# Kernel tuning notes

Measured on AMD Instinct MI355X. Metric: run time of the kernel, lower is better.

The kernel has to match this reference:

```python
import jax, jax.numpy as jnp
import numpy as np

HIDDEN = 128
N_NODES = 100000
N_EDGES = 200000
NEG_SLOPE = 0.01  # torch LeakyReLU default


def setup_inputs() -> dict:
    key = jax.random.key(0)
    ks = jax.random.split(key, 12)
    h = HIDDEN
    lim = 1.0 / np.sqrt(h)
    lim3 = 1.0 / np.sqrt(3 * h)
    u = lambda k, shape, l: jax.random.uniform(k, shape, jnp.float32, -l, l)
    return {
        "x_src": jax.random.normal(ks[0], (N_NODES, h), jnp.float32),
        "x_dst": jax.random.normal(ks[1], (N_NODES, h), jnp.float32),
        "edge_index": jax.random.randint(ks[2], (2, N_EDGES), 0, N_NODES, jnp.int64),
        # parent_encoder Linear(h, h)
        "Wp": u(ks[3], (h, h), lim), "bp": u(ks[4], (h,), lim),
        # child_encoder Linear(h, h)
        "Wc": u(ks[5], (h, h), lim), "bc": u(ks[6], (h,), lim),
        # edge_weight_mlp: Linear(3h, h) -> ReLU -> Linear(h, h)
        "W1": u(ks[7], (h, 3 * h), lim3), "b1": u(ks[8], (h,), lim3),
        "W2": u(ks[9], (h, h), lim), "b2": u(ks[10], (h,), lim),
    }


def reference(x_src, x_dst, edge_index, Wp, bp, Wc, bc, W1, b1, W2, b2):
    # gather node feats per edge  [E, h]
    par = x_src[edge_index[0]]
    cld = x_dst[edge_index[1]]
    # dual encoders: Linear + LeakyReLU (Dropout is identity in eval)
    enc_p = jax.nn.leaky_relu(par @ Wp.T + bp, NEG_SLOPE)
    enc_c = jax.nn.leaky_relu(cld @ Wc.T + bc, NEG_SLOPE)
    diff = jnp.abs(par - cld)
    ef = jnp.concatenate([enc_p, enc_c, diff], axis=-1)  # [E, 3h]
    # edge_weight_mlp
    edge_attr = jax.nn.relu(ef @ W1.T + b1) @ W2.T + b2  # [E, h]
    return edge_attr
```

## Files before the change

### kernel.cpp

```cpp
#include <hip/hip_runtime.h>

typedef unsigned short u16;
typedef __attribute__((ext_vector_type(8))) short v8s;
typedef __attribute__((ext_vector_type(4))) float v4f;
typedef __attribute__((ext_vector_type(4))) float f4;

#define HID 128
#define TM  64
#define EFS 392
#define HS  136
#define FOS 136

__device__ __forceinline__ u16 f2b(float f) {
    union { float f; unsigned u; } v; v.f = f;
    unsigned u = v.u;
    u += 0x7fffu + ((u >> 16) & 1u);
    return (u16)(u >> 16);
}

#define MFMA(A, B, C) __builtin_amdgcn_mfma_f32_16x16x32_bf16(A, B, C, 0, 0, 0)

__global__ void cvt_weights(const float* __restrict__ Wp, const float* __restrict__ Wc,
                            const float* __restrict__ W1, const float* __restrict__ W2,
                            u16* __restrict__ dst)
{
    int i = blockIdx.x * 256 + threadIdx.x;
    const float* s; int off;
    if (i < 4096)       { s = Wp; off = 0; }
    else if (i < 8192)  { s = Wc; off = 4096; }
    else if (i < 20480) { s = W1; off = 8192; }
    else                { s = W2; off = 20480; }
    int j = i - off;
    f4 v = ((const f4*)s)[j];
    u16* d = dst + (size_t)i * 4;
    d[0] = f2b(v[0]); d[1] = f2b(v[1]); d[2] = f2b(v[2]); d[3] = f2b(v[3]);
}

__global__ __launch_bounds__(256, 2) void edge_attr_kernel(
    const float* __restrict__ x_src, const float* __restrict__ x_dst,
    const int* __restrict__ ei,
    const u16* __restrict__ wsW,
    const float* __restrict__ bp, const float* __restrict__ bc,
    const float* __restrict__ b1, const float* __restrict__ b2,
    float* __restrict__ out, int E)
{
    __shared__ __align__(16) u16 sEF[TM * EFS];
    __shared__ __align__(16) u16 sH [TM * HS];

    const u16* wsWp = wsW;
    const u16* wsWc = wsW + 16384;
    const u16* wsW1 = wsW + 32768;
    const u16* wsW2 = wsW + 81920;

    const int t  = threadIdx.x;
    const int e0 = blockIdx.x * TM;
    const int* ei0 = ei;
    const int* ei1 = ei + E;

    #pragma unroll
    for (int i = 0; i < 4; ++i) {
        int idx = t + i * 256;
        int r = idx >> 4;
        int c = (idx & 15) << 3;
        int e = e0 + r; if (e >= E) e = E - 1;
        const f4* ps = (const f4*)(x_src + (size_t)ei0[e] * HID + c);
        const f4* qs = (const f4*)(x_dst + (size_t)ei1[e] * HID + c);
        f4 p0 = ps[0], p1 = ps[1];
        f4 q0 = qs[0], q1 = qs[1];
        v8s pb, qb, db;
        #pragma unroll
        for (int j = 0; j < 4; ++j) {
            pb[j]     = (short)f2b(p0[j]);
            pb[j + 4] = (short)f2b(p1[j]);
            qb[j]     = (short)f2b(q0[j]);
            qb[j + 4] = (short)f2b(q1[j]);
            db[j]     = (short)f2b(fabsf(p0[j] - q0[j]));
            db[j + 4] = (short)f2b(fabsf(p1[j] - q1[j]));
        }
        *(v8s*)&sEF[r * EFS       + c] = pb;
        *(v8s*)&sEF[r * EFS + 128 + c] = qb;
        *(v8s*)&sEF[r * EFS + 256 + c] = db;
    }
    __syncthreads();

    const int lane = t & 63;
    const int ln = lane & 15;
    const int lq = lane >> 4;
    const int n0 = (t >> 6) * 32;

    {
        v8s Bp[2][4], Bc[2][4];
        float bpv[2], bcv[2];
        #pragma unroll
        for (int nt = 0; nt < 2; ++nt) {
            int n = n0 + nt * 16 + ln;
            bpv[nt] = bp[n];
            bcv[nt] = bc[n];
            #pragma unroll
            for (int kt = 0; kt < 4; ++kt) {
                Bp[nt][kt] = *(const v8s*)(wsWp + (size_t)n * HID + kt * 32 + lq * 8);
                Bc[nt][kt] = *(const v8s*)(wsWc + (size_t)n * HID + kt * 32 + lq * 8);
            }
        }
        v4f aP[4][2], aC[4][2];
        #pragma unroll
        for (int mt = 0; mt < 4; ++mt)
            #pragma unroll
            for (int nt = 0; nt < 2; ++nt) {
                aP[mt][nt] = (v4f){0.f, 0.f, 0.f, 0.f};
                aC[mt][nt] = (v4f){0.f, 0.f, 0.f, 0.f};
            }
        #pragma unroll
        for (int mt = 0; mt < 4; ++mt) {
            const int rbase = (mt * 16 + ln) * EFS + lq * 8;
            v8s A[4];
            #pragma unroll
            for (int kt = 0; kt < 4; ++kt) A[kt] = *(const v8s*)&sEF[rbase + kt * 32];
            #pragma unroll
            for (int nt = 0; nt < 2; ++nt)
                #pragma unroll
                for (int kt = 0; kt < 4; ++kt) aP[mt][nt] = MFMA(A[kt], Bp[nt][kt], aP[mt][nt]);
            #pragma unroll
            for (int kt = 0; kt < 4; ++kt) A[kt] = *(const v8s*)&sEF[rbase + 128 + kt * 32];
            #pragma unroll
            for (int nt = 0; nt < 2; ++nt)
                #pragma unroll
                for (int kt = 0; kt < 4; ++kt) aC[mt][nt] = MFMA(A[kt], Bc[nt][kt], aC[mt][nt]);
        }
        __syncthreads();
        #pragma unroll
        for (int mt = 0; mt < 4; ++mt)
            #pragma unroll
            for (int nt = 0; nt < 2; ++nt)
                #pragma unroll
                for (int rg = 0; rg < 4; ++rg) {
                    int row = mt * 16 + lq * 4 + rg;
                    int col = n0 + nt * 16 + ln;
                    float vp = aP[mt][nt][rg] + bpv[nt];
                    vp = vp > 0.f ? vp : 0.01f * vp;
                    sEF[row * EFS + col] = f2b(vp);
                    float vc = aC[mt][nt][rg] + bcv[nt];
                    vc = vc > 0.f ? vc : 0.01f * vc;
                    sEF[row * EFS + 128 + col] = f2b(vc);
                }
        __syncthreads();
    }

    {
        float b1v[2];
        #pragma unroll
        for (int nt = 0; nt < 2; ++nt) b1v[nt] = b1[n0 + nt * 16 + ln];
        v4f acc[4][2];
        #pragma unroll
        for (int mt = 0; mt < 4; ++mt)
            #pragma unroll
            for (int nt = 0; nt < 2; ++nt) acc[mt][nt] = (v4f){0.f, 0.f, 0.f, 0.f};
        #pragma unroll
        for (int ktc = 0; ktc < 3; ++ktc) {
            v8s B[2][4];
            #pragma unroll
            for (int nt = 0; nt < 2; ++nt) {
                int n = n0 + nt * 16 + ln;
                #pragma unroll
                for (int k4 = 0; k4 < 4; ++k4)
                    B[nt][k4] = *(const v8s*)(wsW1 + (size_t)n * 384 + ktc * 128 + k4 * 32 + lq * 8);
            }
            #pragma unroll
            for (int mt = 0; mt < 4; ++mt) {
                const int rbase = (mt * 16 + ln) * EFS + ktc * 128 + lq * 8;
                v8s A[4];
                #pragma unroll
                for (int k4 = 0; k4 < 4; ++k4) A[k4] = *(const v8s*)&sEF[rbase + k4 * 32];
                #pragma unroll
                for (int nt = 0; nt < 2; ++nt)
                    #pragma unroll
                    for (int k4 = 0; k4 < 4; ++k4) acc[mt][nt] = MFMA(A[k4], B[nt][k4], acc[mt][nt]);
            }
        }
        #pragma unroll
        for (int mt = 0; mt < 4; ++mt)
            #pragma unroll
            for (int nt = 0; nt < 2; ++nt)
                #pragma unroll
                for (int rg = 0; rg < 4; ++rg) {
                    int row = mt * 16 + lq * 4 + rg;
                    int col = n0 + nt * 16 + ln;
                    float v = acc[mt][nt][rg] + b1v[nt];
                    sH[row * HS + col] = f2b(fmaxf(v, 0.f));
                }
        __syncthreads();
    }

    {
        float* sF = (float*)sEF;
        v8s B2[2][4];
        float b2v[2];
        #pragma unroll
        for (int nt = 0; nt < 2; ++nt) {
            int n = n0 + nt * 16 + ln;
            b2v[nt] = b2[n];
            #pragma unroll
            for (int kt = 0; kt < 4; ++kt)
                B2[nt][kt] = *(const v8s*)(wsW2 + (size_t)n * HID + kt * 32 + lq * 8);
        }
        v4f acc[4][2];
        #pragma unroll
        for (int mt = 0; mt < 4; ++mt)
            #pragma unroll
            for (int nt = 0; nt < 2; ++nt) acc[mt][nt] = (v4f){0.f, 0.f, 0.f, 0.f};
        #pragma unroll
        for (int mt = 0; mt < 4; ++mt) {
            const int rbase = (mt * 16 + ln) * HS + lq * 8;
            v8s A[4];
            #pragma unroll
            for (int kt = 0; kt < 4; ++kt) A[kt] = *(const v8s*)&sH[rbase + kt * 32];
            #pragma unroll
            for (int nt = 0; nt < 2; ++nt)
                #pragma unroll
                for (int kt = 0; kt < 4; ++kt) acc[mt][nt] = MFMA(A[kt], B2[nt][kt], acc[mt][nt]);
        }
        #pragma unroll
        for (int mt = 0; mt < 4; ++mt)
            #pragma unroll
            for (int nt = 0; nt < 2; ++nt)
                #pragma unroll
                for (int rg = 0; rg < 4; ++rg) {
                    int row = mt * 16 + lq * 4 + rg;
                    int col = n0 + nt * 16 + ln;
                    sF[row * FOS + col] = acc[mt][nt][rg] + b2v[nt];
                }
        __syncthreads();
    }

    {
        const float* sF = (const float*)sEF;
        #pragma unroll
        for (int i = 0; i < 8; ++i) {
            int idx = t + i * 256;
            int r = idx >> 5;
            int c = (idx & 31) << 2;
            int e = e0 + r;
            if (e < E)
                *(f4*)(out + (size_t)e * HID + c) = *(const f4*)&sF[r * FOS + c];
        }
    }
}

extern "C" void kernel_launch(void* const* d_in, const int* in_sizes, int n_in,
                              void* d_out, int out_size, void* d_ws, size_t ws_size,
                              hipStream_t stream) {
    const float* x_src = (const float*)d_in[0];
    const float* x_dst = (const float*)d_in[1];
    const int*   ei    = (const int*)d_in[2];
    const float* Wp    = (const float*)d_in[3];
    const float* bp    = (const float*)d_in[4];
    const float* Wc    = (const float*)d_in[5];
    const float* bc    = (const float*)d_in[6];
    const float* W1    = (const float*)d_in[7];
    const float* b1    = (const float*)d_in[8];
    const float* W2    = (const float*)d_in[9];
    const float* b2    = (const float*)d_in[10];
    float* out = (float*)d_out;
    u16* wsW = (u16*)d_ws;

    int E = in_sizes[2] / 2;

    cvt_weights<<<96, 256, 0, stream>>>(Wp, Wc, W1, W2, wsW);

    int blocks = (E + TM - 1) / TM;
    edge_attr_kernel<<<blocks, 256, 0, stream>>>(
        x_src, x_dst, ei, wsW, bp, bc, b1, b2, out, E);
}
```

Before: 284.8 us.

## Shrink LDS footprint to raise occupancy and write output directly from MFMA accumulators

Reorganises shared memory so the |p-c| diff lives in the hidden buffer, shrinking the LDS tiles. This allows three blocks per CU instead of two, and the launch bound is raised to match. Edge indices are loaded once per lane and broadcast with shuffles instead of being reloaded per row. The final fp32 staging through LDS is dropped in favour of direct scalar global stores, which trades coalesced 16-byte writes for fewer LDS round trips and one fewer barrier. An extra barrier is added before overwriting sH, and register pressure under the tighter launch bound may cause spills.

Measured after the change: 300.1 us. +5.4%, slower.

```diff
diff --git a/kernel.cpp b/kernel.cpp
--- a/kernel.cpp
+++ b/kernel.cpp
@@ -7,9 +7,8 @@
 
 #define HID 128
 #define TM  64
-#define EFS 392
-#define HS  136
-#define FOS 136
+#define SEF_S 260
+#define SH_S  132
 
 __device__ __forceinline__ u16 f2b(float f) {
     union { float f; unsigned u; } v; v.f = f;
@@ -36,7 +35,7 @@
     d[0] = f2b(v[0]); d[1] = f2b(v[1]); d[2] = f2b(v[2]); d[3] = f2b(v[3]);
 }
 
-__global__ __launch_bounds__(256, 2) void edge_attr_kernel(
+__global__ __launch_bounds__(256, 3) void edge_attr_kernel(
     const float* __restrict__ x_src, const float* __restrict__ x_dst,
     const int* __restrict__ ei,
     const u16* __restrict__ wsW,
@@ -44,8 +43,8 @@
     const float* __restrict__ b1, const float* __restrict__ b2,
     float* __restrict__ out, int E)
 {
-    __shared__ __align__(16) u16 sEF[TM * EFS];
-    __shared__ __align__(16) u16 sH [TM * HS];
+    __shared__ __align__(16) u16 sEF[TM * SEF_S];
+    __shared__ __align__(16) u16 sH [TM * SH_S];
 
     const u16* wsWp = wsW;
     const u16* wsWc = wsW + 16384;
@@ -53,18 +52,22 @@
     const u16* wsW2 = wsW + 81920;
 
     const int t  = threadIdx.x;
+    const int l  = t & 63;
     const int e0 = blockIdx.x * TM;
-    const int* ei0 = ei;
-    const int* ei1 = ei + E;
-
+
+    int eg = e0 + l; if (eg >= E) eg = E - 1;
+    const int pidx = ei[eg];
+    const int cidx = ei[E + eg];
+
+    const int cg = (t & 15) << 3;
     #pragma unroll
     for (int i = 0; i < 4; ++i) {
-        int idx = t + i * 256;
-        int r = idx >> 4;
-        int c = (idx & 15) << 3;
-        int e = e0 + r; if (e >= E) e = E - 1;
-        const f4* ps = (const f4*)(x_src + (size_t)ei0[e] * HID + c);
-        const f4* qs = (const f4*)(x_dst + (size_t)ei1[e] * HID + c);
+        int r = (t >> 4) + i * 16;
+        int rl = r & 63;
+        int pi = __shfl(pidx, rl);
+        int ci = __shfl(cidx, rl);
+        const f4* ps = (const f4*)(x_src + (size_t)pi * HID + cg);
+        const f4* qs = (const f4*)(x_dst + (size_t)ci * HID + cg);
         f4 p0 = ps[0], p1 = ps[1];
         f4 q0 = qs[0], q1 = qs[1];
         v8s pb, qb, db;
@@ -77,13 +80,13 @@
             db[j]     = (short)f2b(fabsf(p0[j] - q0[j]));
             db[j + 4] = (short)f2b(fabsf(p1[j] - q1[j]));
         }
-        *(v8s*)&sEF[r * EFS       + c] = pb;
-        *(v8s*)&sEF[r * EFS + 128 + c] = qb;
-        *(v8s*)&sEF[r * EFS + 256 + c] = db;
+        *(v8s*)&sEF[r * SEF_S       + cg] = pb;
+        *(v8s*)&sEF[r * SEF_S + 128 + cg] = qb;
+        *(v8s*)&sH [r * SH_S        + cg] = db;
     }
     __syncthreads();
 
-    const int lane = t & 63;
+    const int lane = l;
     const int ln = lane & 15;
     const int lq = lane >> 4;
     const int n0 = (t >> 6) * 32;
@@ -112,7 +115,7 @@
             }
         #pragma unroll
         for (int mt = 0; mt < 4; ++mt) {
-            const int rbase = (mt * 16 + ln) * EFS + lq * 8;
+            const int rbase = (mt * 16 + ln) * SEF_S + lq * 8;
             v8s A[4];
             #pragma unroll
             for (int kt = 0; kt < 4; ++kt) A[kt] = *(const v8s*)&sEF[rbase + kt * 32];
@@ -138,10 +141,10 @@
                     int col = n0 + nt * 16 + ln;
                     float vp = aP[mt][nt][rg] + bpv[nt];
                     vp = vp > 0.f ? vp : 0.01f * vp;
-                    sEF[row * EFS + col] = f2b(vp);
+                    sEF[row * SEF_S + col] = f2b(vp);
                     float vc = aC[mt][nt][rg] + bcv[nt];
                     vc = vc > 0.f ? vc : 0.01f * vc;
-                    sEF[row * EFS + 128 + col] = f2b(vc);
+                    sEF[row * SEF_S + 128 + col] = f2b(vc);
                 }
         __syncthreads();
     }
@@ -165,18 +168,21 @@
                 for (int k4 = 0; k4 < 4; ++k4)
                     B[nt][k4] = *(const v8s*)(wsW1 + (size_t)n * 384 + ktc * 128 + k4 * 32 + lq * 8);
             }
+            const u16* Asrc = (ktc < 2) ? (sEF + ktc * 128) : sH;
+            const int  Astr = (ktc < 2) ? SEF_S : SH_S;
             #pragma unroll
             for (int mt = 0; mt < 4; ++mt) {
-                const int rbase = (mt * 16 + ln) * EFS + ktc * 128 + lq * 8;
+                const int rbase = (mt * 16 + ln) * Astr + lq * 8;
                 v8s A[4];
                 #pragma unroll
-                for (int k4 = 0; k4 < 4; ++k4) A[k4] = *(const v8s*)&sEF[rbase + k4 * 32];
+                for (int k4 = 0; k4 < 4; ++k4) A[k4] = *(const v8s*)&Asrc[rbase + k4 * 32];
                 #pragma unroll
                 for (int nt = 0; nt < 2; ++nt)
                     #pragma unroll
                     for (int k4 = 0; k4 < 4; ++k4) acc[mt][nt] = MFMA(A[k4], B[nt][k4], acc[mt][nt]);
             }
         }
+        __syncthreads();
         #pragma unroll
         for (int mt = 0; mt < 4; ++mt)
             #pragma unroll
@@ -186,13 +192,12 @@
                     int row = mt * 16 + lq * 4 + rg;
                     int col = n0 + nt * 16 + ln;
                     float v = acc[mt][nt][rg] + b1v[nt];
-                    sH[row * HS + col] = f2b(fmaxf(v, 0.f));
+                    sH[row * SH_S + col] = f2b(fmaxf(v, 0.f));
                 }
         __syncthreads();
     }
 
     {
-        float* sF = (float*)sEF;
         v8s B2[2][4];
         float b2v[2];
         #pragma unroll
@@ -210,7 +215,7 @@
             for (int nt = 0; nt < 2; ++nt) acc[mt][nt] = (v4f){0.f, 0.f, 0.f, 0.f};
         #pragma unroll
         for (int mt = 0; mt < 4; ++mt) {
-            const int rbase = (mt * 16 + ln) * HS + lq * 8;
+            const int rbase = (mt * 16 + ln) * SH_S + lq * 8;
             v8s A[4];
             #pragma unroll
             for (int kt = 0; kt < 4; ++kt) A[kt] = *(const v8s*)&sH[rbase + kt * 32];
@@ -226,23 +231,10 @@
                 #pragma unroll
                 for (int rg = 0; rg < 4; ++rg) {
                     int row = mt * 16 + lq * 4 + rg;
-                    int col = n0 + nt * 16 + ln;
-                    sF[row * FOS + col] = acc[mt][nt][rg] + b2v[nt];
+                    int e = e0 + row;
+                    if (e < E)
+                        out[(size_t)e * HID + n0 + nt * 16 + ln] = acc[mt][nt][rg] + b2v[nt];
                 }
-        __syncthreads();
-    }
-
-    {
-        const float* sF = (const float*)sEF;
-        #pragma unroll
-        for (int i = 0; i < 8; ++i) {
-            int idx = t + i * 256;
-            int r = idx >> 5;
-            int c = (idx & 31) << 2;
-            int e = e0 + r;
-            if (e < E)
-                *(f4*)(out + (size_t)e * HID + c) = *(const f4*)&sF[r * FOS + c];
-        }
     }
 }
 
```
